# Performance work log

Hardware: AMD Instinct MI355X
Metric: run time of the kernel (lower is better)

## Reference

```python
import jax, jax.numpy as jnp
import numpy as np

V0, V1, C = 64, 128, 128
V = V0 * V1  # product-graph node count = kron eigenvalue count


def setup_inputs() -> dict:
    key = jax.random.key(0)
    ks = jax.random.split(key, 8)
    x = jax.random.normal(ks[0], (V, C), dtype=jnp.float32)
    edge_index = jax.random.randint(ks[1], (2, 100), 0, V)  # unused on spectral path
    L = jnp.zeros((2, 2), dtype=jnp.float32)                # unused on spectral path
    mass = jax.random.uniform(ks[2], (V,), dtype=jnp.float32) + 0.5  # positive lumped mass
    evals0 = jax.random.uniform(ks[3], (V0,), dtype=jnp.float32) * 2.0  # factor-graph eigenvalues >= 0
    evals1 = jax.random.uniform(ks[4], (V1,), dtype=jnp.float32) * 2.0
    evecs = jax.random.normal(ks[5], (V, V), dtype=jnp.float32) / np.float32(np.sqrt(V))
    diffusion_time = jax.random.uniform(ks[6], (2, C), dtype=jnp.float32)  # nn.Parameter [P, C_inout]
    return {
        "x": x, "edge_index": edge_index, "L": L, "mass": mass,
        "evals0": evals0, "evals1": evals1, "evecs": evecs,
        "diffusion_time": diffusion_time,
    }


def reference(x, edge_index, L, mass, evals0, evals1, evecs, diffusion_time):
    # to_basis: project mass-weighted signal onto the spectral basis. [V,C]
    x_spec = evecs.T @ (x * mass[:, None])
    # Per-channel Kronecker diffusion coefficients:
    # kron(exp(-t0[c]*evals0), exp(-t1[c]*evals1)) for each channel c.
    e0 = jnp.exp(-evals0[:, None] * diffusion_time[0][None, :])  # [V0, C]
    e1 = jnp.exp(-evals1[:, None] * diffusion_time[1][None, :])  # [V1, C]
    diffusion_coefs = (e0[:, None, :] * e1[None, :, :]).reshape(V0 * V1, C)  # [V, C]
    # from_basis: back to node domain.
    x_diffuse = evecs @ (diffusion_coefs * x_spec)
    return x_diffuse
```

## Files before the change

### kernel.cpp

```cpp
#include <hip/hip_runtime.h>
#include <hip/hip_bf16.h>
#include <stdint.h>

#define V 8192
#define C 128
#define KS 8
#define KCH (V / KS)
#define BK 64

typedef __attribute__((ext_vector_type(8))) short short8;
typedef __attribute__((ext_vector_type(4))) float floatx4;

typedef unsigned int __attribute__((address_space(1))) gas_u32;
typedef unsigned int __attribute__((address_space(3))) las_u32;
#define GLD16(g, l) __builtin_amdgcn_global_load_lds((const gas_u32*)(g), (las_u32*)(l), 16, 0, 0)

static __device__ __forceinline__ unsigned short f2bf(float f) {
    unsigned u = __float_as_uint(f);
    u += 0x7FFF + ((u >> 16) & 1);
    return (unsigned short)(u >> 16);
}

__global__ __launch_bounds__(256) void prep_xmt(const float* __restrict__ x,
                                                const float* __restrict__ mass,
                                                unsigned short* __restrict__ XMT) {
    __shared__ float tile[64][65];
    const int k0 = blockIdx.x * 64;
    const int c0 = blockIdx.y * 64;
    const int t = threadIdx.x;
#pragma unroll
    for (int p = 0; p < 16; ++p) {
        int idx = p * 256 + t;
        int kk = idx >> 6, cc = idx & 63;
        tile[kk][cc] = x[(size_t)(k0 + kk) * C + (c0 + cc)] * mass[k0 + kk];
    }
    __syncthreads();
#pragma unroll
    for (int p = 0; p < 16; ++p) {
        int idx = p * 256 + t;
        int cc = idx >> 6, kk = idx & 63;
        XMT[(size_t)(c0 + cc) * V + (k0 + kk)] = f2bf(tile[kk][cc]);
    }
}

__global__ __launch_bounds__(256, 3) void gemm1_fused(const unsigned short* __restrict__ XMT,
                                                      const float* __restrict__ E,
                                                      float* __restrict__ P1) {
    __shared__ __align__(16) unsigned short ldsA[128 * BK];
    __shared__ __align__(16) unsigned short ldsB[128 * BK];
    const int bx = blockIdx.x;
    const int ks = bx & (KS - 1);
    const int n0 = (bx >> 3) * 128;
    const int kb = ks * KCH;
    const int t = threadIdx.x;
    const int w = t >> 6;
    const int lane = t & 63;
    const int q = lane >> 4;
    const int l15 = lane & 15;
    const int wm = (w & 1) * 64;
    const int wn = (w >> 1) * 64;
    const int srow = lane >> 3;
    const int spos = lane & 7;
    const int vg = t & 7;
    const int jg = t >> 3;

    floatx4 acc[4][4] = {};

    for (int k0 = kb; k0 < kb + KCH; k0 += BK) {
        __syncthreads();
#pragma unroll
        for (int j = 0; j < 4; ++j) {
            int r = 32 * w + 8 * j + srow;
            int cp = spos ^ (r & 7);
            GLD16(&XMT[(size_t)r * V + k0 + 8 * cp], &ldsA[(32 * w + 8 * j) * BK]);
        }
        float4 ld[8];
#pragma unroll
        for (int rr = 0; rr < 8; ++rr)
            ld[rr] = *(const float4*)&E[(size_t)(k0 + vg * 8 + rr) * V + n0 + jg * 4];
        const float* lf = (const float*)ld;
#pragma unroll
        for (int jj = 0; jj < 4; ++jj) {
            int j = jg * 4 + jj;
            int phys = vg ^ (j & 7);
            short8 b;
#pragma unroll
            for (int rr = 0; rr < 8; ++rr) b[rr] = (short)f2bf(lf[rr * 4 + jj]);
            *(short8*)&ldsB[j * BK + phys * 8] = b;
        }
        __syncthreads();
#pragma unroll
        for (int kk = 0; kk < BK; kk += 32) {
            short8 af[4], bf[4];
#pragma unroll
            for (int mi = 0; mi < 4; ++mi) {
                int m = wm + mi * 16 + l15;
                int cpos = ((kk >> 3) + q) ^ (m & 7);
                af[mi] = *(const short8*)&ldsA[m * BK + 8 * cpos];
            }
#pragma unroll
            for (int ni = 0; ni < 4; ++ni) {
                int n = wn + ni * 16 + l15;
                int cpos = ((kk >> 3) + q) ^ (n & 7);
                bf[ni] = *(const short8*)&ldsB[n * BK + 8 * cpos];
            }
#pragma unroll
            for (int mi = 0; mi < 4; ++mi)
#pragma unroll
                for (int ni = 0; ni < 4; ++ni)
                    acc[mi][ni] = __builtin_amdgcn_mfma_f32_16x16x32_bf16(af[mi], bf[ni], acc[mi][ni], 0, 0, 0);
        }
    }
    float* Pks = P1 + (size_t)ks * C * V;
#pragma unroll
    for (int mi = 0; mi < 4; ++mi) {
        int mrow = wm + mi * 16 + q * 4;
#pragma unroll
        for (int ni = 0; ni < 4; ++ni) {
            int n = n0 + wn + ni * 16 + l15;
#pragma unroll
            for (int r = 0; r < 4; ++r)
                Pks[(size_t)(mrow + r) * V + n] = acc[mi][ni][r];
        }
    }
}

__global__ __launch_bounds__(256, 3) void gemm2_fused(const float* __restrict__ E,
                                                      const unsigned short* __restrict__ YT,
                                                      float* __restrict__ P2) {
    __shared__ __align__(16) unsigned short ldsA[128 * BK];
    __shared__ __align__(16) unsigned short ldsB[128 * BK];
    const int bx = blockIdx.x;
    const int ks = bx & (KS - 1);
    const int m0 = (bx >> 3) * 128;
    const int kb = ks * KCH;
    const int t = threadIdx.x;
    const int w = t >> 6;
    const int lane = t & 63;
    const int q = lane >> 4;
    const int l15 = lane & 15;
    const int wm = (w & 1) * 64;
    const int wn = (w >> 1) * 64;
    const int srow = lane >> 3;
    const int spos = lane & 7;
    const int r16 = t >> 2;
    const int p = t & 3;

    floatx4 acc[4][4] = {};

    for (int k0 = kb; k0 < kb + KCH; k0 += BK) {
        __syncthreads();
#pragma unroll
        for (int j = 0; j < 4; ++j) {
            int r = 32 * w + 8 * j + srow;
            int cp = spos ^ (r & 7);
            GLD16(&YT[(size_t)r * V + k0 + 8 * cp], &ldsB[(32 * w + 8 * j) * BK]);
        }
#pragma unroll
        for (int half = 0; half < 2; ++half) {
            int row = r16 + half * 64;
            float4 la[4];
#pragma unroll
            for (int u = 0; u < 4; ++u)
                la[u] = *(const float4*)&E[(size_t)(m0 + row) * V + k0 + p * 16 + u * 4];
            const float* lf = (const float*)la;
#pragma unroll
            for (int cc = 0; cc < 2; ++cc) {
                int phys = (2 * p + cc) ^ (row & 7);
                short8 av;
#pragma unroll
                for (int e = 0; e < 8; ++e) av[e] = (short)f2bf(lf[cc * 8 + e]);
                *(short8*)&ldsA[row * BK + phys * 8] = av;
            }
        }
        __syncthreads();
#pragma unroll
        for (int kk = 0; kk < BK; kk += 32) {
            short8 af[4], bf[4];
#pragma unroll
            for (int mi = 0; mi < 4; ++mi) {
                int m = wm + mi * 16 + l15;
                int cpos = ((kk >> 3) + q) ^ (m & 7);
                af[mi] = *(const short8*)&ldsA[m * BK + 8 * cpos];
            }
#pragma unroll
            for (int ni = 0; ni < 4; ++ni) {
                int n = wn + ni * 16 + l15;
                int cpos = ((kk >> 3) + q) ^ (n & 7);
                bf[ni] = *(const short8*)&ldsB[n * BK + 8 * cpos];
            }
#pragma unroll
            for (int mi = 0; mi < 4; ++mi)
#pragma unroll
                for (int ni = 0; ni < 4; ++ni)
                    acc[mi][ni] = __builtin_amdgcn_mfma_f32_16x16x32_bf16(af[mi], bf[ni], acc[mi][ni], 0, 0, 0);
        }
    }
    float* Pks = P2 + (size_t)ks * V * C;
#pragma unroll
    for (int mi = 0; mi < 4; ++mi) {
        int mrow = m0 + wm + mi * 16 + q * 4;
#pragma unroll
        for (int ni = 0; ni < 4; ++ni) {
            int n = wn + ni * 16 + l15;
#pragma unroll
            for (int r = 0; r < 4; ++r)
                Pks[(size_t)(mrow + r) * C + n] = acc[mi][ni][r];
        }
    }
}

__global__ __launch_bounds__(256) void red1(const float* __restrict__ P1,
                                            const float* __restrict__ ev0,
                                            const float* __restrict__ ev1,
                                            const float* __restrict__ dt,
                                            unsigned short* __restrict__ YT) {
    int id = blockIdx.x * 256 + threadIdx.x;
    int c = id >> 10;
    int j0 = (id & 1023) * 8;
    float s[8] = {};
#pragma unroll
    for (int ks = 0; ks < KS; ++ks) {
        const float* row = &P1[((size_t)ks * C + c) * V + j0];
        float4 a = *(const float4*)row;
        float4 b = *(const float4*)(row + 4);
        s[0] += a.x; s[1] += a.y; s[2] += a.z; s[3] += a.w;
        s[4] += b.x; s[5] += b.y; s[6] += b.z; s[7] += b.w;
    }
    float t0 = dt[c], t1 = dt[C + c];
    float a0 = ev0[j0 >> 7] * t0;
    short8 yv;
#pragma unroll
    for (int jj = 0; jj < 8; ++jj) {
        float coef = __expf(-(a0 + ev1[(j0 + jj) & 127] * t1));
        yv[jj] = (short)f2bf(s[jj] * coef);
    }
    *(short8*)&YT[(size_t)c * V + j0] = yv;
}

__global__ __launch_bounds__(256) void red2(const float* __restrict__ P2,
                                            float* __restrict__ out) {
    int id = blockIdx.x * 256 + threadIdx.x;
    size_t off = (size_t)id * 4;
    float4 s = {0.f, 0.f, 0.f, 0.f};
#pragma unroll
    for (int ks = 0; ks < KS; ++ks) {
        float4 v = *(const float4*)&P2[(size_t)ks * V * C + off];
        s.x += v.x; s.y += v.y; s.z += v.z; s.w += v.w;
    }
    *(float4*)&out[off] = s;
}

extern "C" void kernel_launch(void* const* d_in, const int* in_sizes, int n_in,
                              void* d_out, int out_size, void* d_ws, size_t ws_size,
                              hipStream_t stream) {
    const float* x    = (const float*)d_in[0];
    const float* mass = (const float*)d_in[3];
    const float* ev0  = (const float*)d_in[4];
    const float* ev1  = (const float*)d_in[5];
    const float* E    = (const float*)d_in[6];
    const float* dt   = (const float*)d_in[7];
    float* out = (float*)d_out;

    unsigned short* XMT = (unsigned short*)d_ws;
    unsigned short* YT  = XMT + (size_t)V * C;
    float* P = (float*)(YT + (size_t)V * C);

    prep_xmt<<<dim3(V / 64, C / 64), 256, 0, stream>>>(x, mass, XMT);
    gemm1_fused<<<(V / 128) * KS, 256, 0, stream>>>(XMT, E, P);
    red1<<<(C * V / 8) / 256, 256, 0, stream>>>(P, ev0, ev1, dt, YT);
    gemm2_fused<<<(V / 128) * KS, 256, 0, stream>>>(E, YT, P);
    red2<<<(V * C / 4) / 256, 256, 0, stream>>>(P, out);
}
```

Baseline: 464.7 us.

## Software-pipeline fp32 evecs loads via register double buffering in both GEMMs

Both split-K GEMM kernels now prefetch the next fp32 evecs tile into registers while the current one is converted to bf16 and consumed, unrolling the K loop by two with alternating register buffers. The global_load_lds direct-to-LDS path for the bf16 operand is replaced by plain vector loads into registers followed by swizzled LDS stores. Launch bounds drop from 3 to 2 waves per SIMD to make room for the extra registers. The aim is to hide global-load latency behind MFMA work, at the cost of occupancy and an extra register round trip for the bf16 operand.

```diff
diff --git a/kernel.cpp b/kernel.cpp
--- a/kernel.cpp
+++ b/kernel.cpp
@@ -7,13 +7,10 @@
 #define KS 8
 #define KCH (V / KS)
 #define BK 64
+#define NI (KCH / BK)
 
 typedef __attribute__((ext_vector_type(8))) short short8;
 typedef __attribute__((ext_vector_type(4))) float floatx4;
-
-typedef unsigned int __attribute__((address_space(1))) gas_u32;
-typedef unsigned int __attribute__((address_space(3))) las_u32;
-#define GLD16(g, l) __builtin_amdgcn_global_load_lds((const gas_u32*)(g), (las_u32*)(l), 16, 0, 0)
 
 static __device__ __forceinline__ unsigned short f2bf(float f) {
     unsigned u = __float_as_uint(f);
@@ -43,7 +40,33 @@
     }
 }
 
-__global__ __launch_bounds__(256, 3) void gemm1_fused(const unsigned short* __restrict__ XMT,
+#define MFMA_BODY                                                                   \
+    {                                                                               \
+        _Pragma("unroll")                                                           \
+        for (int kk = 0; kk < BK; kk += 32) {                                       \
+            short8 af[4], bf[4];                                                    \
+            _Pragma("unroll")                                                       \
+            for (int mi = 0; mi < 4; ++mi) {                                        \
+                int m = wm + mi * 16 + l15;                                         \
+                int cpos = ((kk >> 3) + q) ^ (m & 7);                               \
+                af[mi] = *(const short8*)&ldsA[m * BK + 8 * cpos];                  \
+            }                                                                       \
+            _Pragma("unroll")                                                       \
+            for (int ni = 0; ni < 4; ++ni) {                                        \
+                int n = wn + ni * 16 + l15;                                         \
+                int cpos = ((kk >> 3) + q) ^ (n & 7);                               \
+                bf[ni] = *(const short8*)&ldsB[n * BK + 8 * cpos];                  \
+            }                                                                       \
+            _Pragma("unroll")                                                       \
+            for (int mi = 0; mi < 4; ++mi)                                          \
+                _Pragma("unroll")                                                   \
+                for (int ni = 0; ni < 4; ++ni)                                      \
+                    acc[mi][ni] = __builtin_amdgcn_mfma_f32_16x16x32_bf16(          \
+                        af[mi], bf[ni], acc[mi][ni], 0, 0, 0);                      \
+        }                                                                           \
+    }
+
+__global__ __launch_bounds__(256, 2) void gemm1_fused(const unsigned short* __restrict__ XMT,
                                                       const float* __restrict__ E,
                                                       float* __restrict__ P1) {
     __shared__ __align__(16) unsigned short ldsA[128 * BK];
@@ -53,63 +76,74 @@
     const int n0 = (bx >> 3) * 128;
     const int kb = ks * KCH;
     const int t = threadIdx.x;
-    const int w = t >> 6;
-    const int lane = t & 63;
-    const int q = lane >> 4;
-    const int l15 = lane & 15;
-    const int wm = (w & 1) * 64;
-    const int wn = (w >> 1) * 64;
-    const int srow = lane >> 3;
-    const int spos = lane & 7;
-    const int vg = t & 7;
-    const int jg = t >> 3;
+    const int w = t >> 6, lane = t & 63, q = lane >> 4, l15 = lane & 15;
+    const int wm = (w & 1) * 64, wn = (w >> 1) * 64;
+    const int a_row = t >> 1;
+    const int a_c0 = (t & 1) * 4;
+    const int vg = t & 7, jg = t >> 3;
 
     floatx4 acc[4][4] = {};
-
-    for (int k0 = kb; k0 < kb + KCH; k0 += BK) {
-        __syncthreads();
-#pragma unroll
-        for (int j = 0; j < 4; ++j) {
-            int r = 32 * w + 8 * j + srow;
-            int cp = spos ^ (r & 7);
-            GLD16(&XMT[(size_t)r * V + k0 + 8 * cp], &ldsA[(32 * w + 8 * j) * BK]);
-        }
-        float4 ld[8];
+    float4 e0[8], e1[8];
+
+#pragma unroll
+    for (int rr = 0; rr < 8; ++rr)
+        e0[rr] = *(const float4*)&E[(size_t)(kb + vg * 8 + rr) * V + n0 + jg * 4];
+
+    for (int it = 0; it < NI; it += 2) {
+        const int k0 = kb + it * BK;
+        const int k1 = k0 + BK;
+        const int kp = (k1 + BK < kb + KCH) ? (k1 + BK) : (kb + KCH - BK);
+        __syncthreads();
+        uint4 br[4];
+#pragma unroll
+        for (int u = 0; u < 4; ++u)
+            br[u] = *(const uint4*)&XMT[(size_t)a_row * V + k0 + 8 * (a_c0 + u)];
 #pragma unroll
         for (int rr = 0; rr < 8; ++rr)
-            ld[rr] = *(const float4*)&E[(size_t)(k0 + vg * 8 + rr) * V + n0 + jg * 4];
-        const float* lf = (const float*)ld;
-#pragma unroll
-        for (int jj = 0; jj < 4; ++jj) {
-            int j = jg * 4 + jj;
-            int phys = vg ^ (j & 7);
-            short8 b;
-#pragma unroll
-            for (int rr = 0; rr < 8; ++rr) b[rr] = (short)f2bf(lf[rr * 4 + jj]);
-            *(short8*)&ldsB[j * BK + phys * 8] = b;
-        }
-        __syncthreads();
-#pragma unroll
-        for (int kk = 0; kk < BK; kk += 32) {
-            short8 af[4], bf[4];
-#pragma unroll
-            for (int mi = 0; mi < 4; ++mi) {
-                int m = wm + mi * 16 + l15;
-                int cpos = ((kk >> 3) + q) ^ (m & 7);
-                af[mi] = *(const short8*)&ldsA[m * BK + 8 * cpos];
+            e1[rr] = *(const float4*)&E[(size_t)(k1 + vg * 8 + rr) * V + n0 + jg * 4];
+#pragma unroll
+        for (int u = 0; u < 4; ++u) {
+            int c = a_c0 + u;
+            *(uint4*)&ldsA[a_row * BK + ((c ^ (a_row & 7))) * 8] = br[u];
+        }
+        {
+            const float* lf = (const float*)e0;
+#pragma unroll
+            for (int jj = 0; jj < 4; ++jj) {
+                int j = jg * 4 + jj;
+                short8 b;
+#pragma unroll
+                for (int rr = 0; rr < 8; ++rr) b[rr] = (short)f2bf(lf[rr * 4 + jj]);
+                *(short8*)&ldsB[j * BK + (vg ^ (j & 7)) * 8] = b;
             }
-#pragma unroll
-            for (int ni = 0; ni < 4; ++ni) {
-                int n = wn + ni * 16 + l15;
-                int cpos = ((kk >> 3) + q) ^ (n & 7);
-                bf[ni] = *(const short8*)&ldsB[n * BK + 8 * cpos];
+        }
+        __syncthreads();
+        MFMA_BODY;
+        __syncthreads();
+#pragma unroll
+        for (int u = 0; u < 4; ++u)
+            br[u] = *(const uint4*)&XMT[(size_t)a_row * V + k1 + 8 * (a_c0 + u)];
+#pragma unroll
+        for (int rr = 0; rr < 8; ++rr)
+            e0[rr] = *(const float4*)&E[(size_t)(kp + vg * 8 + rr) * V + n0 + jg * 4];
+#pragma unroll
+        for (int u = 0; u < 4; ++u) {
+            int c = a_c0 + u;
+            *(uint4*)&ldsA[a_row * BK + ((c ^ (a_row & 7))) * 8] = br[u];
+        }
+        {
+            const float* lf = (const float*)e1;
+#pragma unroll
+            for (int jj = 0; jj < 4; ++jj) {
+                int j = jg * 4 + jj;
+                short8 b;
+#pragma unroll
+                for (int rr = 0; rr < 8; ++rr) b[rr] = (short)f2bf(lf[rr * 4 + jj]);
+                *(short8*)&ldsB[j * BK + (vg ^ (j & 7)) * 8] = b;
             }
-#pragma unroll
-            for (int mi = 0; mi < 4; ++mi)
-#pragma unroll
-                for (int ni = 0; ni < 4; ++ni)
-                    acc[mi][ni] = __builtin_amdgcn_mfma_f32_16x16x32_bf16(af[mi], bf[ni], acc[mi][ni], 0, 0, 0);
-        }
+        }
+        __syncthreads();
+        MFMA_BODY;
     }
     float* Pks = P1 + (size_t)ks * C * V;
 #pragma unroll
@@ -125,7 +159,7 @@
     }
 }
 
-__global__ __launch_bounds__(256, 3) void gemm2_fused(const float* __restrict__ E,
+__global__ __launch_bounds__(256, 2) void gemm2_fused(const float* __restrict__ E,
                                                       const unsigned short* __restrict__ YT,
                                                       float* __restrict__ P2) {
     __shared__ __align__(16) unsigned short ldsA[128 * BK];
@@ -135,66 +169,88 @@
     const int m0 = (bx >> 3) * 128;
     const int kb = ks * KCH;
     const int t = threadIdx.x;
-    const int w = t >> 6;
-    const int lane = t & 63;
-    const int q = lane >> 4;
-    const int l15 = lane & 15;
-    const int wm = (w & 1) * 64;
-    const int wn = (w >> 1) * 64;
-    const int srow = lane >> 3;
-    const int spos = lane & 7;
-    const int r16 = t >> 2;
-    const int p = t & 3;
+    const int w = t >> 6, lane = t & 63, q = lane >> 4, l15 = lane & 15;
+    const int wm = (w & 1) * 64, wn = (w >> 1) * 64;
+    const int r16 = t >> 2, p = t & 3;
+    const int b_row = t >> 1;
+    const int b_c0 = (t & 1) * 4;
 
     floatx4 acc[4][4] = {};
-
-    for (int k0 = kb; k0 < kb + KCH; k0 += BK) {
-        __syncthreads();
-#pragma unroll
-        for (int j = 0; j < 4; ++j) {
-            int r = 32 * w + 8 * j + srow;
-            int cp = spos ^ (r & 7);
-            GLD16(&YT[(size_t)r * V + k0 + 8 * cp], &ldsB[(32 * w + 8 * j) * BK]);
-        }
-#pragma unroll
-        for (int half = 0; half < 2; ++half) {
-            int row = r16 + half * 64;
-            float4 la[4];
+    float4 e0[8], e1[8];
+
+#pragma unroll
+    for (int half = 0; half < 2; ++half)
+#pragma unroll
+        for (int u = 0; u < 4; ++u)
+            e0[half * 4 + u] = *(const float4*)&E[(size_t)(m0 + r16 + half * 64) * V + kb + p * 16 + u * 4];
+
+    for (int it = 0; it < NI; it += 2) {
+        const int k0 = kb + it * BK;
+        const int k1 = k0 + BK;
+        const int kp = (k1 + BK < kb + KCH) ? (k1 + BK) : (kb + KCH - BK);
+        __syncthreads();
+        uint4 br[4];
+#pragma unroll
+        for (int u = 0; u < 4; ++u)
+            br[u] = *(const uint4*)&YT[(size_t)b_row * V + k0 + 8 * (b_c0 + u)];
+#pragma unroll
+        for (int half = 0; half < 2; ++half)
 #pragma unroll
             for (int u = 0; u < 4; ++u)
-                la[u] = *(const float4*)&E[(size_t)(m0 + row) * V + k0 + p * 16 + u * 4];
-            const float* lf = (const float*)la;
-#pragma unroll
-            for (int cc = 0; cc < 2; ++cc) {
-                int phys = (2 * p + cc) ^ (row & 7);
-                short8 av;
-#pragma unroll
-                for (int e = 0; e < 8; ++e) av[e] = (short)f2bf(lf[cc * 8 + e]);
-                *(short8*)&ldsA[row * BK + phys * 8] = av;
+                e1[half * 4 + u] = *(const float4*)&E[(size_t)(m0 + r16 + half * 64) * V + k1 + p * 16 + u * 4];
+#pragma unroll
+        for (int u = 0; u < 4; ++u) {
+            int c = b_c0 + u;
+            *(uint4*)&ldsB[b_row * BK + ((c ^ (b_row & 7))) * 8] = br[u];
+        }
+        {
+            const float* lf = (const float*)e0;
+#pragma unroll
+            for (int half = 0; half < 2; ++half) {
+                int row = r16 + half * 64;
+#pragma unroll
+                for (int cc = 0; cc < 2; ++cc) {
+                    int c = 2 * p + cc;
+                    short8 av;
+#pragma unroll
+                    for (int e = 0; e < 8; ++e) av[e] = (short)f2bf(lf[half * 16 + cc * 8 + e]);
+                    *(short8*)&ldsA[row * BK + ((c ^ (row & 7))) * 8] = av;
+                }
             }
         }
         __syncthreads();
-#pragma unroll
-        for (int kk = 0; kk < BK; kk += 32) {
-            short8 af[4], bf[4];
-#pragma unroll
-            for (int mi = 0; mi < 4; ++mi) {
-                int m = wm + mi * 16 + l15;
-                int cpos = ((kk >> 3) + q) ^ (m & 7);
-                af[mi] = *(const short8*)&ldsA[m * BK + 8 * cpos];
+        MFMA_BODY;
+        __syncthreads();
+#pragma unroll
+        for (int u = 0; u < 4; ++u)
+            br[u] = *(const uint4*)&YT[(size_t)b_row * V + k1 + 8 * (b_c0 + u)];
+#pragma unroll
+        for (int half = 0; half < 2; ++half)
+#pragma unroll
+            for (int u = 0; u < 4; ++u)
+                e0[half * 4 + u] = *(const float4*)&E[(size_t)(m0 + r16 + half * 64) * V + kp + p * 16 + u * 4];
+#pragma unroll
+        for (int u = 0; u < 4; ++u) {
+            int c = b_c0 + u;
+            *(uint4*)&ldsB[b_row * BK + ((c ^ (b_row & 7))) * 8] = br[u];
+        }
+        {
+            const float* lf = (const float*)e1;
+#pragma unroll
+            for (int half = 0; half < 2; ++half) {
+                int row = r16 + half * 64;
+#pragma unroll
+                for (int cc = 0; cc < 2; ++cc) {
+                    int c = 2 * p + cc;
+                    short8 av;
+#pragma unroll
+                    for (int e = 0; e < 8; ++e) av[e] = (short)f2bf(lf[half * 16 + cc * 8 + e]);
+                    *(short8*)&ldsA[row * BK + ((c ^ (row & 7))) * 8] = av;
+                }
             }
-#pragma unroll
-            for (int ni = 0; ni < 4; ++ni) {
-                int n = wn + ni * 16 + l15;
-                int cpos = ((kk >> 3) + q) ^ (n & 7);
-                bf[ni] = *(const short8*)&ldsB[n * BK + 8 * cpos];
-            }
-#pragma unroll
-            for (int mi = 0; mi < 4; ++mi)
-#pragma unroll
-                for (int ni = 0; ni < 4; ++ni)
-                    acc[mi][ni] = __builtin_amdgcn_mfma_f32_16x16x32_bf16(af[mi], bf[ni], acc[mi][ni], 0, 0, 0);
-        }
+        }
+        __syncthreads();
+        MFMA_BODY;
     }
     float* Pks = P2 + (size_t)ks * V * C;
 #pragma unroll
```

After: 457.1 us. Within noise of the previous version (-1.6%).
